# Optimization experiments

Measured on AMD Instinct MI355X. Metric: run time of the kernel, lower is better.

## Reference

```python
import jax, jax.numpy as jnp
import numpy as np
from jax import lax

N_QUBITS = 8
DIM = 256  # 2**8 amplitudes
NUM_BLOCKS = 16
DEPTH = 1
ALPHA = 0.5
BATCH = 512

# Z-sign tables: qubit 0 is the most-significant bit of the flattened state index
_bits = (np.arange(DIM)[:, None] >> (N_QUBITS - 1 - np.arange(N_QUBITS))) & 1  # (256, 8)
_SIGNS = jnp.asarray(1.0 - 2.0 * _bits, dtype=jnp.float32)  # (256, 8)
_pairs = [(i, j) for i in range(N_QUBITS) for j in range(i + 1, N_QUBITS)]
_PAIR_SIGNS = jnp.stack([_SIGNS[:, i] * _SIGNS[:, j] for (i, j) in _pairs], axis=1)  # (256, 28)


def _apply_ry(state, c, s, q):
    # state: (N, 256) real (RY and CNOT keep the state real); gate on qubit q
    dl, dr = 2 ** q, 2 ** (N_QUBITS - 1 - q)
    st = state.reshape(-1, dl, 2, dr)
    s0, s1 = st[:, :, 0, :], st[:, :, 1, :]
    c_, s_ = c[:, None, None], s[:, None, None]
    n0 = c_ * s0 - s_ * s1
    n1 = s_ * s0 + c_ * s1
    return jnp.stack([n0, n1], axis=2).reshape(-1, DIM)


def _apply_cnot_chain(state, i):
    # CNOT control=i, target=i+1 (adjacent qubits)
    dl, dr = 2 ** i, 2 ** (N_QUBITS - 2 - i)
    st = state.reshape(-1, dl, 2, 2, dr)
    c0 = st[:, :, 0]                  # control=0: unchanged
    c1 = st[:, :, 1][:, :, ::-1]      # control=1: flip target bit
    return jnp.stack([c0, c1], axis=2).reshape(-1, DIM)


def _quantum_map(theta):
    # theta: (N, 8) -> (N, 36) [Z_i expectations (8) then Z_i Z_j for i<j (28)]
    half = 0.5 * theta
    c, s = jnp.cos(half), jnp.sin(half)
    state = jnp.zeros((theta.shape[0], DIM), dtype=theta.dtype).at[:, 0].set(1.0)
    for q in range(N_QUBITS):
        state = _apply_ry(state, c[:, q], s[:, q], q)
    for _ in range(DEPTH):
        for i in range(N_QUBITS - 1):
            state = _apply_cnot_chain(state, i)
    p = state * state  # probabilities (state is real)
    single = p @ _SIGNS          # (N, 8)
    two_body = p @ _PAIR_SIGNS   # (N, 28)
    return jnp.concatenate([single, two_body], axis=1)


def _bn(x, g, b, m, v):
    # inference-mode BatchNorm2d, eps=1e-5
    inv = g / jnp.sqrt(v + 1e-5)
    return x * inv[None, :, None, None] + (b - m * inv)[None, :, None, None]


def _conv(x, w, b):
    y = lax.conv_general_dilated(x, w, (1, 1), 'SAME',
                                 dimension_numbers=('NCHW', 'OIHW', 'NCHW'))
    return y + b[None, :, None, None]


def _maxpool2(x):
    return lax.reduce_window(x, -jnp.inf, lax.max, (1, 1, 2, 2), (1, 1, 2, 2), 'VALID')


def setup_inputs() -> dict:
    key = jax.random.key(0)
    ks = jax.random.split(key, 8)
    f32 = jnp.float32
    return {
        'x': jax.random.normal(ks[0], (BATCH, 3, 64, 64), dtype=f32),
        'conv1_w': jax.random.normal(ks[1], (16, 3, 3, 3), dtype=f32) * 0.1,
        'conv1_b': jnp.zeros((16,), f32),
        'bn1_g': jnp.ones((16,), f32), 'bn1_b': jnp.zeros((16,), f32),
        'bn1_m': jnp.zeros((16,), f32), 'bn1_v': jnp.ones((16,), f32),
        'conv2_w': jax.random.normal(ks[2], (32, 16, 3, 3), dtype=f32) * 0.08,
        'conv2_b': jnp.zeros((32,), f32),
        'bn2_g': jnp.ones((32,), f32), 'bn2_b': jnp.zeros((32,), f32),
        'bn2_m': jnp.zeros((32,), f32), 'bn2_v': jnp.ones((32,), f32),
        'conv3_w': jax.random.normal(ks[3], (64, 32, 3, 3), dtype=f32) * 0.06,
        'conv3_b': jnp.zeros((64,), f32),
        'bn3_g': jnp.ones((64,), f32), 'bn3_b': jnp.zeros((64,), f32),
        'bn3_m': jnp.zeros((64,), f32), 'bn3_v': jnp.ones((64,), f32),
        'proj_w': jax.random.normal(ks[4], (NUM_BLOCKS, 256, N_QUBITS), dtype=f32) * 0.06,
        'proj_b': jnp.zeros((NUM_BLOCKS, N_QUBITS), f32),
        'cls_w': jax.random.normal(ks[5], (10, NUM_BLOCKS * 36), dtype=f32) * 0.04,
        'cls_b': jnp.zeros((10,), f32),
    }


def reference(x, conv1_w, conv1_b, bn1_g, bn1_b, bn1_m, bn1_v,
              conv2_w, conv2_b, bn2_g, bn2_b, bn2_m, bn2_v,
              conv3_w, conv3_b, bn3_g, bn3_b, bn3_m, bn3_v,
              proj_w, proj_b, cls_w, cls_b):
    h = _maxpool2(jax.nn.relu(_bn(_conv(x, conv1_w, conv1_b), bn1_g, bn1_b, bn1_m, bn1_v)))
    h = _maxpool2(jax.nn.relu(_bn(_conv(h, conv2_w, conv2_b), bn2_g, bn2_b, bn2_m, bn2_v)))
    h = _maxpool2(jax.nn.relu(_bn(_conv(h, conv3_w, conv3_b), bn3_g, bn3_b, bn3_m, bn3_v)))
    B = h.shape[0]
    feats = h.reshape(B, NUM_BLOCKS, 256)  # 16 chunks of 256
    z = jnp.einsum('bkc,kcd->bkd', feats, proj_w) + proj_b[None]  # (B, 16, 8)
    theta = ALPHA * jnp.tanh(z)
    q_out = _quantum_map(theta.reshape(B * NUM_BLOCKS, N_QUBITS))  # (B*16, 36)
    combined = q_out.reshape(B, NUM_BLOCKS * 36)
    return combined @ cls_w.T + cls_b
```

## Files before the change

### kernel.cpp

```cpp
#include <hip/hip_runtime.h>
#include <hip/hip_bf16.h>
#include <math.h>

typedef __attribute__((ext_vector_type(8))) short short8;
typedef __attribute__((ext_vector_type(4))) float f32x4;

__device__ __forceinline__ unsigned short f2bf(float f) {
    union { float f; unsigned u; } x; x.f = f;
    unsigned r = x.u + 0x7FFF + ((x.u >> 16) & 1);
    return (unsigned short)(r >> 16);
}

__device__ __forceinline__ short8 mk8(uint2 a, uint2 b) {
    union { uint2 u[2]; short8 s; } x;
    x.u[0] = a; x.u[1] = b;
    return x.s;
}

__device__ __forceinline__ short8 mk8u(unsigned a, unsigned b, unsigned c, unsigned d) {
    union { unsigned u[4]; short8 s; } x;
    x.u[0] = a; x.u[1] = b; x.u[2] = c; x.u[3] = d;
    return x.s;
}

__global__ void k_prep(const float* __restrict__ w2, const float* __restrict__ w3,
    const float* g2, const float* be2, const float* m2, const float* v2, const float* cb2,
    const float* g3, const float* be3, const float* m3, const float* v3, const float* cb3,
    const float* __restrict__ w1,
    const float* g1, const float* be1, const float* m1, const float* v1, const float* cb1,
    const float* __restrict__ pjw,
    unsigned short* __restrict__ wp2, unsigned short* __restrict__ wp3,
    unsigned short* __restrict__ wp1,
    float* __restrict__ cst2, float* __restrict__ cst3, float* __restrict__ cst1,
    float* __restrict__ pjwt)
{
    int tid = blockIdx.x * 256 + threadIdx.x;
    if (tid < 5120) {
        int j = tid & 7, lane = (tid >> 3) & 63, o = (tid >> 9) & 1, s = tid >> 10;
        int kl = ((lane >> 4) << 3) + j;
        int tp = s * 2 + (kl >> 4);
        int ic = kl & 15;
        int oc = o * 16 + (lane & 15);
        float val = (tp < 9) ? w2[(oc * 16 + ic) * 9 + tp] : 0.f;
        wp2[tid] = f2bf(val);
    } else if (tid < 23552) {
        int idx = tid - 5120;
        int j = idx & 7, lane = (idx >> 3) & 63, o = (idx >> 9) & 3, tap = idx >> 11;
        int ic = ((lane >> 4) << 3) + j;
        int oc = o * 16 + (lane & 15);
        wp3[idx] = f2bf(w3[(oc * 32 + ic) * 9 + tap]);
    } else if (tid < 23648) {
        int c = tid - 23552;
        if (c < 32) {
            float inv = g2[c] * rsqrtf(v2[c] + 1e-5f);
            cst2[c] = inv;
            cst2[32 + c] = (cb2[c] - m2[c]) * inv + be2[c];
        } else {
            int c3 = c - 32;
            float inv = g3[c3] * rsqrtf(v3[c3] + 1e-5f);
            cst3[c3] = inv;
            cst3[64 + c3] = (cb3[c3] - m3[c3]) * inv + be3[c3];
        }
    } else if (tid < 24672) {
        int idx = tid - 23648;
        int j = idx & 7, lane = (idx >> 3) & 63, s = (idx >> 9) & 1;
        int k = ((lane >> 4) << 3) + j;
        int oc = lane & 15;
        float val = 0.f;
        if (s == 0) {
            int tap = k >> 2, ic = k & 3;
            if (ic < 3) val = w1[(oc * 3 + ic) * 9 + tap];
        } else {
            if (k < 3) val = w1[(oc * 3 + k) * 9 + 8];
        }
        wp1[idx] = f2bf(val);
    } else if (tid < 24688) {
        int c = tid - 24672;
        float inv = g1[c] * rsqrtf(v1[c] + 1e-5f);
        cst1[c] = inv;
        cst1[16 + c] = (cb1[c] - m1[c]) * inv + be1[c];
    } else if (tid < 57456) {
        int idx = tid - 24688;
        int k = idx >> 11, d = (idx >> 8) & 7, c = idx & 255;
        pjwt[idx] = pjw[k * 2048 + c * 8 + d];
    }
}

__global__ __launch_bounds__(256, 2) void k_fused(
    const float* __restrict__ x,
    const unsigned short* __restrict__ wp1, const float* __restrict__ cst1,
    const unsigned short* __restrict__ wp2, const float* __restrict__ cst2,
    const unsigned short* __restrict__ wp3, const float* __restrict__ cst3,
    const float* __restrict__ pjwt, const float* __restrict__ pjb,
    const float* __restrict__ cw, const float* __restrict__ cbias,
    float* __restrict__ out)
{
    __shared__ __align__(16) unsigned char smem[62784];
    unsigned short* xs  = (unsigned short*)smem;
    unsigned short* h2t = (unsigned short*)smem;
    unsigned short* h1  = (unsigned short*)(smem + 25920);
    float* feats = (float*)(smem + 25920);
    float* czs   = (float*)(smem + 25920 + 17408);
    float* partl = czs + 128;

    int b = blockIdx.x, t = threadIdx.x;
    int lane = t & 63, w = t >> 6, q = lane >> 4, xl = lane & 15;
    const float* img = x + (size_t)b * 12288;

    short8 A10 = *(const short8*)(wp1 + (lane << 3));
    short8 A11 = *(const short8*)(wp1 + ((64 + lane) << 3));
    int t0 = 2 * q, t1 = 2 * q + 1;
    int dy0 = t0 / 3 - 1, dx0 = t0 % 3 - 1;
    int dy1 = t1 / 3 - 1, dx1 = t1 % 3 - 1;
    float inv1[4], bs1[4];
    #pragma unroll
    for (int reg = 0; reg < 4; ++reg) {
        inv1[reg] = cst1[q * 4 + reg];
        bs1[reg]  = cst1[16 + q * 4 + reg];
    }
    #pragma unroll 1
    for (int h = 0; h < 2; ++h) {
        if (h) __syncthreads();
        int y0 = h * 32 - 1;
        #pragma unroll 1
        for (int i = 0; i < 9; ++i) {
            int idx = t + i * 256;
            if (idx < 2244) {
                int y = idx / 66, xx = idx - y * 66;
                int gy = y0 + y, gx = xx - 1;
                float v0 = 0.f, v1 = 0.f, v2 = 0.f;
                if ((unsigned)gy < 64u && (unsigned)gx < 64u) {
                    const float* pb = img + gy * 64 + gx;
                    v0 = pb[0]; v1 = pb[4096]; v2 = pb[8192];
                }
                uint2 pk;
                pk.x = (unsigned)f2bf(v0) | ((unsigned)f2bf(v1) << 16);
                pk.y = (unsigned)f2bf(v2);
                ((uint2*)xs)[idx] = pk;
            }
        }
        __syncthreads();
        #pragma unroll 1
        for (int xT = 0; xT < 4; ++xT) {
            int xb = xT * 16 + xl + 1;
            float pv[4], vo[4];
            #pragma unroll
            for (int r = 0; r < 8; ++r) {
                int ly = w * 8 + r + 1;
                const uint2* base = (const uint2*)xs;
                uint2 ua = base[(ly + dy0) * 66 + xb + dx0];
                uint2 ub = base[(ly + dy1) * 66 + xb + dx1];
                uint2 uc = base[(ly + 1) * 66 + xb + 1];
                f32x4 acc = (f32x4){0.f, 0.f, 0.f, 0.f};
                acc = __builtin_amdgcn_mfma_f32_16x16x32_bf16(A10, mk8(ua, ub), acc, 0, 0, 0);
                acc = __builtin_amdgcn_mfma_f32_16x16x32_bf16(A11, mk8(uc, uc), acc, 0, 0, 0);
                #pragma unroll
                for (int reg = 0; reg < 4; ++reg) {
                    float val = fmaxf(acc[reg] * inv1[reg] + bs1[reg], 0.f);
                    if (r & 1) {
                        float vm = fmaxf(val, pv[reg]);
                        vo[reg] = fmaxf(vm, __shfl_xor(vm, 1, 64));
                    } else {
                        pv[reg] = val;
                    }
                }
                if ((r & 1) && !(lane & 1)) {
                    int py = h * 16 + w * 4 + (r >> 1);
                    int px = xT * 8 + (xl >> 1);
                    int pos = py * 32 + px;
                    unsigned u0 = (unsigned)f2bf(vo[0]) | ((unsigned)f2bf(vo[1]) << 16);
                    unsigned u1 = (unsigned)f2bf(vo[2]) | ((unsigned)f2bf(vo[3]) << 16);
                    unsigned* hp = (unsigned*)h1 + pos * 9 + q * 2;
                    hp[0] = u0; hp[1] = u1;
                }
            }
        }
    }
    __syncthreads();

    if (t < 68) {
        int y, xx;
        if (t < 18)      { y = 0;       xx = t; }
        else if (t < 36) { y = 17;      xx = t - 18; }
        else if (t < 52) { y = t - 35;  xx = 0; }
        else             { y = t - 51;  xx = 17; }
        uint4* p = (uint4*)(h2t + (y * 18 + xx) * 40);
        uint4 z = {0u, 0u, 0u, 0u};
        p[0] = z; p[1] = z; p[2] = z; p[3] = z; p[4] = z;
    }
    short8 A2[5][2];
    #pragma unroll
    for (int s = 0; s < 5; ++s)
        #pragma unroll
        for (int o = 0; o < 2; ++o)
            A2[s][o] = *(const short8*)(wp2 + (((s * 2 + o) * 64 + lane) << 3));
    int dyA[5], dxA[5];
    #pragma unroll
    for (int s = 0; s < 5; ++s) {
        int tp = s * 2 + (q >> 1); if (tp > 8) tp = 8;
        int d3 = tp / 3;
        dyA[s] = d3 - 1; dxA[s] = tp - d3 * 3 - 1;
    }
    #pragma unroll 1
    for (int rr = 0; rr < 2; ++rr) {
        f32x4 acc[4][2][2];
        #pragma unroll
        for (int r = 0; r < 4; ++r)
            #pragma unroll
            for (int xT = 0; xT < 2; ++xT)
                #pragma unroll
                for (int o = 0; o < 2; ++o)
                    acc[r][xT][o] = (f32x4){0.f, 0.f, 0.f, 0.f};
        #pragma unroll
        for (int r = 0; r < 4; ++r) {
            int ry = w * 8 + rr * 4 + r;
            #pragma unroll
            for (int xT = 0; xT < 2; ++xT) {
                int gxb = xT * 16 + xl;
                #pragma unroll
                for (int s = 0; s < 5; ++s) {
                    int gy = ry + dyA[s], gx = gxb + dxA[s];
                    bool ok = ((unsigned)gy < 32u) && ((unsigned)gx < 32u);
                    int pos = ok ? gy * 32 + gx : 0;
                    const unsigned* hp = (const unsigned*)h1 + pos * 9 + (q & 1) * 4;
                    unsigned u0 = hp[0], u1 = hp[1], u2 = hp[2], u3 = hp[3];
                    if (!ok) { u0 = 0; u1 = 0; u2 = 0; u3 = 0; }
                    short8 B = mk8u(u0, u1, u2, u3);
                    acc[r][xT][0] = __builtin_amdgcn_mfma_f32_16x16x32_bf16(A2[s][0], B, acc[r][xT][0], 0, 0, 0);
                    acc[r][xT][1] = __builtin_amdgcn_mfma_f32_16x16x32_bf16(A2[s][1], B, acc[r][xT][1], 0, 0, 0);
                }
            }
        }
        #pragma unroll
        for (int oT = 0; oT < 2; ++oT)
            #pragma unroll
            for (int rp = 0; rp < 2; ++rp)
                #pragma unroll
                for (int xT = 0; xT < 2; ++xT) {
                    float vo[4];
                    #pragma unroll
                    for (int reg = 0; reg < 4; ++reg) {
                        int oc = oT * 16 + q * 4 + reg;
                        float inv = cst2[oc], bs = cst2[32 + oc];
                        float v0 = fmaxf(acc[rp * 2][xT][oT][reg] * inv + bs, 0.f);
                        float v1 = fmaxf(acc[rp * 2 + 1][xT][oT][reg] * inv + bs, 0.f);
                        float vm = fmaxf(v0, v1);
                        vo[reg] = fmaxf(vm, __shfl_xor(vm, 1, 64));
                    }
                    if (!(lane & 1)) {
                        int py = w * 4 + rr * 2 + rp;
                        int px = xT * 8 + (xl >> 1);
                        int pos = (py + 1) * 18 + (px + 1);
                        unsigned u0 = (unsigned)f2bf(vo[0]) | ((unsigned)f2bf(vo[1]) << 16);
                        unsigned u1 = (unsigned)f2bf(vo[2]) | ((unsigned)f2bf(vo[3]) << 16);
                        unsigned* hp = (unsigned*)h2t + pos * 20 + oT * 8 + q * 2;
                        hp[0] = u0; hp[1] = u1;
                    }
                }
    }
    __syncthreads();

    #pragma unroll 1
    for (int op = 0; op < 2; ++op) {
        short8 A3[9][2];
        #pragma unroll
        for (int tap = 0; tap < 9; ++tap)
            #pragma unroll
            for (int tt = 0; tt < 2; ++tt)
                A3[tap][tt] = *(const short8*)(wp3 + (((tap * 4 + op * 2 + tt) * 64 + lane) << 3));
        f32x4 acc[4][2];
        #pragma unroll
        for (int r = 0; r < 4; ++r) {
            acc[r][0] = (f32x4){0.f, 0.f, 0.f, 0.f};
            acc[r][1] = (f32x4){0.f, 0.f, 0.f, 0.f};
        }
        #pragma unroll
        for (int r = 0; r < 4; ++r) {
            int ry = w * 4 + r + 1;
            #pragma unroll
            for (int tap = 0; tap < 9; ++tap) {
                int pos = (ry + tap / 3 - 1) * 18 + xl + (tap % 3);
                short8 B = *(const short8*)(h2t + pos * 40 + q * 8);
                acc[r][0] = __builtin_amdgcn_mfma_f32_16x16x32_bf16(A3[tap][0], B, acc[r][0], 0, 0, 0);
                acc[r][1] = __builtin_amdgcn_mfma_f32_16x16x32_bf16(A3[tap][1], B, acc[r][1], 0, 0, 0);
            }
        }
        #pragma unroll
        for (int tt = 0; tt < 2; ++tt)
            #pragma unroll
            for (int reg = 0; reg < 4; ++reg) {
                int oc = (op * 2 + tt) * 16 + q * 4 + reg;
                float inv = cst3[oc], bs = cst3[64 + oc];
                #pragma unroll
                for (int rp = 0; rp < 2; ++rp) {
                    float v0 = fmaxf(acc[rp * 2][tt][reg] * inv + bs, 0.f);
                    float v1 = fmaxf(acc[rp * 2 + 1][tt][reg] * inv + bs, 0.f);
                    float vm = fmaxf(v0, v1);
                    float vv = fmaxf(vm, __shfl_xor(vm, 1, 64));
                    if (!(lane & 1))
                        feats[oc * 68 + (w * 2 + rp) * 8 + (xl >> 1)] = vv;
                }
            }
    }
    __syncthreads();

    if (t < 128) {
        int k = t >> 3, d = t & 7;
        const float4* wrow = (const float4*)(pjwt + (k * 8 + d) * 256);
        float zacc = 0.f;
        #pragma unroll 4
        for (int i = 0; i < 64; ++i) {
            int c4 = (i + k) & 63;
            float4 wv = wrow[c4];
            const float* fp = &feats[(k * 4 + (c4 >> 4)) * 68 + 4 * (c4 & 15)];
            float4 fv = *(const float4*)fp;
            zacc = fmaf(wv.x, fv.x, zacc);
            zacc = fmaf(wv.y, fv.y, zacc);
            zacc = fmaf(wv.z, fv.z, zacc);
            zacc = fmaf(wv.w, fv.w, zacc);
        }
        float z = zacc + pjb[k * 8 + d];
        czs[k * 8 + d] = cosf(0.5f * tanhf(z));
    }
    __syncthreads();
    if (t < 160) {
        int k = t / 10, c = t - (t / 10) * 10;
        float cz[8];
        #pragma unroll
        for (int i = 0; i < 8; ++i) cz[i] = czs[k * 8 + i];
        const float* cwp = cw + c * 576 + k * 36;
        float s = 0.f;
        float pp = 1.f;
        #pragma unroll
        for (int i = 0; i < 8; ++i) { pp *= cz[i]; s = fmaf(pp, cwp[i], s); }
        int cnt = 8;
        #pragma unroll
        for (int i = 0; i < 8; ++i) {
            float p2 = 1.f;
            #pragma unroll
            for (int j = i + 1; j < 8; ++j) { p2 *= cz[j]; s = fmaf(p2, cwp[cnt++], s); }
        }
        partl[k * 10 + c] = s;
    }
    __syncthreads();
    if (t < 10) {
        float s = cbias[t];
        #pragma unroll
        for (int k = 0; k < 16; ++k) s += partl[k * 10 + t];
        out[b * 10 + t] = s;
    }
}

extern "C" void kernel_launch(void* const* d_in, const int* in_sizes, int n_in,
                              void* d_out, int out_size, void* d_ws, size_t ws_size,
                              hipStream_t stream) {
    const float* x     = (const float*)d_in[0];
    const float* c1w   = (const float*)d_in[1];
    const float* c1b   = (const float*)d_in[2];
    const float* b1g   = (const float*)d_in[3];
    const float* b1b   = (const float*)d_in[4];
    const float* b1m   = (const float*)d_in[5];
    const float* b1v   = (const float*)d_in[6];
    const float* c2w   = (const float*)d_in[7];
    const float* c2b   = (const float*)d_in[8];
    const float* b2g   = (const float*)d_in[9];
    const float* b2b   = (const float*)d_in[10];
    const float* b2m   = (const float*)d_in[11];
    const float* b2v   = (const float*)d_in[12];
    const float* c3w   = (const float*)d_in[13];
    const float* c3b   = (const float*)d_in[14];
    const float* b3g   = (const float*)d_in[15];
    const float* b3b   = (const float*)d_in[16];
    const float* b3m   = (const float*)d_in[17];
    const float* b3v   = (const float*)d_in[18];
    const float* pjw   = (const float*)d_in[19];
    const float* pjb   = (const float*)d_in[20];
    const float* cw    = (const float*)d_in[21];
    const float* cbias = (const float*)d_in[22];
    float* outp = (float*)d_out;

    unsigned char* prep = (unsigned char*)d_ws;
    unsigned short* wp2 = (unsigned short*)prep;
    unsigned short* wp3 = (unsigned short*)(prep + 16384);
    unsigned short* wp1 = (unsigned short*)(prep + 16384 + 36864);
    float* cst2 = (float*)(prep + 16384 + 36864 + 2048);
    float* cst3 = cst2 + 64;
    float* cst1 = cst3 + 128;
    float* pjwt = (float*)(prep + 16384 + 36864 + 2048 + 1024);

    k_prep<<<225, 256, 0, stream>>>(c2w, c3w, b2g, b2b, b2m, b2v, c2b,
                                    b3g, b3b, b3m, b3v, c3b,
                                    c1w, b1g, b1b, b1m, b1v, c1b, pjw,
                                    wp2, wp3, wp1, cst2, cst3, cst1, pjwt);
    k_fused<<<512, 256, 0, stream>>>(x, wp1, cst1, wp2, cst2, wp3, cst3,
                                     pjwt, pjb, cw, cbias, outp);
}
```

Measured before the change: 147.1 us.

## Double threads per block and split padded LDS activations into halves

The fused CNN kernel now runs 512 threads (8 waves) per image instead of 256. Each wave handles half the rows in conv1 and conv2, and in conv3 the output-channel halves are split across waves. The h1 and h2 activation buffers are re-laid out as two zero-padded halves, each 16 bytes per position, so conv2 no longer needs bounds checks or per-element selects when loading. This adds parallelism and latency hiding per image, but launch_bounds(512,4) limits registers per thread, which could cause spills given the large A2/A3 fragment arrays.

```diff
diff --git a/kernel.cpp b/kernel.cpp
--- a/kernel.cpp
+++ b/kernel.cpp
@@ -14,12 +14,6 @@
 __device__ __forceinline__ short8 mk8(uint2 a, uint2 b) {
     union { uint2 u[2]; short8 s; } x;
     x.u[0] = a; x.u[1] = b;
-    return x.s;
-}
-
-__device__ __forceinline__ short8 mk8u(unsigned a, unsigned b, unsigned c, unsigned d) {
-    union { unsigned u[4]; short8 s; } x;
-    x.u[0] = a; x.u[1] = b; x.u[2] = c; x.u[3] = d;
     return x.s;
 }
 
@@ -86,7 +80,7 @@
     }
 }
 
-__global__ __launch_bounds__(256, 2) void k_fused(
+__global__ __launch_bounds__(512, 4) void k_fused(
     const float* __restrict__ x,
     const unsigned short* __restrict__ wp1, const float* __restrict__ cst1,
     const unsigned short* __restrict__ wp2, const float* __restrict__ cst2,
@@ -95,17 +89,30 @@
     const float* __restrict__ cw, const float* __restrict__ cbias,
     float* __restrict__ out)
 {
-    __shared__ __align__(16) unsigned char smem[62784];
-    unsigned short* xs  = (unsigned short*)smem;
-    unsigned short* h2t = (unsigned short*)smem;
-    unsigned short* h1  = (unsigned short*)(smem + 25920);
-    float* feats = (float*)(smem + 25920);
-    float* czs   = (float*)(smem + 25920 + 17408);
+    __shared__ __align__(16) unsigned char smem[57728];
+    unsigned short* xs   = (unsigned short*)smem;
+    unsigned short* h2tA = (unsigned short*)smem;
+    unsigned short* h2tB = (unsigned short*)(smem + 10368);
+    unsigned short* h1A  = (unsigned short*)(smem + 20736);
+    unsigned short* h1B  = (unsigned short*)(smem + 39232);
+    float* feats = (float*)(smem + 20736);
+    float* czs   = (float*)(smem + 20736 + 17408);
     float* partl = czs + 128;
 
     int b = blockIdx.x, t = threadIdx.x;
     int lane = t & 63, w = t >> 6, q = lane >> 4, xl = lane & 15;
     const float* img = x + (size_t)b * 12288;
+
+    if (t < 264) {
+        int arr = t & 1, idx = t >> 1;
+        int y, xx;
+        if (idx < 34)       { y = 0;        xx = idx; }
+        else if (idx < 68)  { y = 33;       xx = idx - 34; }
+        else if (idx < 100) { y = idx - 67; xx = 0; }
+        else                { y = idx - 99; xx = 33; }
+        uint4 z = {0u, 0u, 0u, 0u};
+        *(uint4*)((arr ? h1B : h1A) + (y * 34 + xx) * 8) = z;
+    }
 
     short8 A10 = *(const short8*)(wp1 + (lane << 3));
     short8 A11 = *(const short8*)(wp1 + ((64 + lane) << 3));
@@ -118,13 +125,14 @@
         inv1[reg] = cst1[q * 4 + reg];
         bs1[reg]  = cst1[16 + q * 4 + reg];
     }
+    unsigned* h1w = (unsigned*)(q < 2 ? h1A : h1B);
     #pragma unroll 1
     for (int h = 0; h < 2; ++h) {
         if (h) __syncthreads();
         int y0 = h * 32 - 1;
         #pragma unroll 1
-        for (int i = 0; i < 9; ++i) {
-            int idx = t + i * 256;
+        for (int i = 0; i < 5; ++i) {
+            int idx = t + i * 512;
             if (idx < 2244) {
                 int y = idx / 66, xx = idx - y * 66;
                 int gy = y0 + y, gx = xx - 1;
@@ -145,8 +153,8 @@
             int xb = xT * 16 + xl + 1;
             float pv[4], vo[4];
             #pragma unroll
-            for (int r = 0; r < 8; ++r) {
-                int ly = w * 8 + r + 1;
+            for (int r = 0; r < 4; ++r) {
+                int ly = w * 4 + r + 1;
                 const uint2* base = (const uint2*)xs;
                 uint2 ua = base[(ly + dy0) * 66 + xb + dx0];
                 uint2 ub = base[(ly + dy1) * 66 + xb + dx1];
@@ -165,12 +173,12 @@
                     }
                 }
                 if ((r & 1) && !(lane & 1)) {
-                    int py = h * 16 + w * 4 + (r >> 1);
+                    int py = h * 16 + w * 2 + (r >> 1);
                     int px = xT * 8 + (xl >> 1);
-                    int pos = py * 32 + px;
+                    int pos = (py + 1) * 34 + (px + 1);
                     unsigned u0 = (unsigned)f2bf(vo[0]) | ((unsigned)f2bf(vo[1]) << 16);
                     unsigned u1 = (unsigned)f2bf(vo[2]) | ((unsigned)f2bf(vo[3]) << 16);
-                    unsigned* hp = (unsigned*)h1 + pos * 9 + q * 2;
+                    unsigned* hp = h1w + pos * 4 + (q & 1) * 2;
                     hp[0] = u0; hp[1] = u1;
                 }
             }
@@ -178,15 +186,20 @@
     }
     __syncthreads();
 
-    if (t < 68) {
+    if (t < 264) {
+        int idx = t >> 1, half = t & 1;
         int y, xx;
-        if (t < 18)      { y = 0;       xx = t; }
-        else if (t < 36) { y = 17;      xx = t - 18; }
-        else if (t < 52) { y = t - 35;  xx = 0; }
-        else             { y = t - 51;  xx = 17; }
-        uint4* p = (uint4*)(h2t + (y * 18 + xx) * 40);
-        uint4 z = {0u, 0u, 0u, 0u};
-        p[0] = z; p[1] = z; p[2] = z; p[3] = z; p[4] = z;
+        if (idx < 18)      { y = 0;        xx = idx; }
+        else if (idx < 36) { y = 17;       xx = idx - 18; }
+        else if (idx < 52) { y = idx - 35; xx = 0; }
+        else if (idx < 68) { y = idx - 51; xx = 17; }
+        else { y = -1; xx = 0; }
+        if (y >= 0) {
+            uint4 z = {0u, 0u, 0u, 0u};
+            int pos = y * 18 + xx;
+            *(uint4*)((half ? h2tB : h2tA) + pos * 16) = z;
+            *(uint4*)((half ? h2tB : h2tA) + pos * 16 + 8) = z;
+        }
     }
     short8 A2[5][2];
     #pragma unroll
@@ -201,8 +214,8 @@
         int d3 = tp / 3;
         dyA[s] = d3 - 1; dxA[s] = tp - d3 * 3 - 1;
     }
-    #pragma unroll 1
-    for (int rr = 0; rr < 2; ++rr) {
+    {
+        const unsigned short* h1r = (q & 1) ? h1B : h1A;
         f32x4 acc[4][2][2];
         #pragma unroll
         for (int r = 0; r < 4; ++r)
@@ -213,19 +226,14 @@
                     acc[r][xT][o] = (f32x4){0.f, 0.f, 0.f, 0.f};
         #pragma unroll
         for (int r = 0; r < 4; ++r) {
-            int ry = w * 8 + rr * 4 + r;
+            int ry = w * 4 + r;
             #pragma unroll
             for (int xT = 0; xT < 2; ++xT) {
                 int gxb = xT * 16 + xl;
                 #pragma unroll
                 for (int s = 0; s < 5; ++s) {
-                    int gy = ry + dyA[s], gx = gxb + dxA[s];
-                    bool ok = ((unsigned)gy < 32u) && ((unsigned)gx < 32u);
-                    int pos = ok ? gy * 32 + gx : 0;
-                    const unsigned* hp = (const unsigned*)h1 + pos * 9 + (q & 1) * 4;
-                    unsigned u0 = hp[0], u1 = hp[1], u2 = hp[2], u3 = hp[3];
-                    if (!ok) { u0 = 0; u1 = 0; u2 = 0; u3 = 0; }
-                    short8 B = mk8u(u0, u1, u2, u3);
+                    int pos = (ry + dyA[s] + 1) * 34 + (gxb + dxA[s] + 1);
+                    short8 B = *(const short8*)(h1r + pos * 8);
                     acc[r][xT][0] = __builtin_amdgcn_mfma_f32_16x16x32_bf16(A2[s][0], B, acc[r][xT][0], 0, 0, 0);
                     acc[r][xT][1] = __builtin_amdgcn_mfma_f32_16x16x32_bf16(A2[s][1], B, acc[r][xT][1], 0, 0, 0);
                 }
@@ -248,20 +256,21 @@
                         vo[reg] = fmaxf(vm, __shfl_xor(vm, 1, 64));
                     }
                     if (!(lane & 1)) {
-                        int py = w * 4 + rr * 2 + rp;
+                        int py = w * 2 + rp;
                         int px = xT * 8 + (xl >> 1);
                         int pos = (py + 1) * 18 + (px + 1);
                         unsigned u0 = (unsigned)f2bf(vo[0]) | ((unsigned)f2bf(vo[1]) << 16);
                         unsigned u1 = (unsigned)f2bf(vo[2]) | ((unsigned)f2bf(vo[3]) << 16);
-                        unsigned* hp = (unsigned*)h2t + pos * 20 + oT * 8 + q * 2;
+                        unsigned* hp = (unsigned*)(oT ? h2tB : h2tA) + pos * 8 + q * 2;
                         hp[0] = u0; hp[1] = u1;
                     }
                 }
     }
     __syncthreads();
 
-    #pragma unroll 1
-    for (int op = 0; op < 2; ++op) {
+    {
+        int op = w & 1, rg = w >> 1;
+        const unsigned short* h2r = (q < 2) ? h2tA : h2tB;
         short8 A3[9][2];
         #pragma unroll
         for (int tap = 0; tap < 9; ++tap)
@@ -276,11 +285,11 @@
         }
         #pragma unroll
         for (int r = 0; r < 4; ++r) {
-            int ry = w * 4 + r + 1;
+            int ry = rg * 4 + r + 1;
             #pragma unroll
             for (int tap = 0; tap < 9; ++tap) {
                 int pos = (ry + tap / 3 - 1) * 18 + xl + (tap % 3);
-                short8 B = *(const short8*)(h2t + pos * 40 + q * 8);
+                short8 B = *(const short8*)(h2r + pos * 16 + (q & 1) * 8);
                 acc[r][0] = __builtin_amdgcn_mfma_f32_16x16x32_bf16(A3[tap][0], B, acc[r][0], 0, 0, 0);
                 acc[r][1] = __builtin_amdgcn_mfma_f32_16x16x32_bf16(A3[tap][1], B, acc[r][1], 0, 0, 0);
             }
@@ -298,7 +307,7 @@
                     float vm = fmaxf(v0, v1);
                     float vv = fmaxf(vm, __shfl_xor(vm, 1, 64));
                     if (!(lane & 1))
-                        feats[oc * 68 + (w * 2 + rp) * 8 + (xl >> 1)] = vv;
+                        feats[oc * 68 + (rg * 2 + rp) * 8 + (xl >> 1)] = vv;
                 }
             }
     }
@@ -392,6 +401,6 @@
                                     b3g, b3b, b3m, b3v, c3b,
                                     c1w, b1g, b1b, b1m, b1v, c1b, pjw,
                                     wp2, wp3, wp1, cst2, cst3, cst1, pjwt);
-    k_fused<<<512, 256, 0, stream>>>(x, wp1, cst1, wp2, cst2, wp3, cst3,
+    k_fused<<<512, 512, 0, stream>>>(x, wp1, cst1, wp2, cst2, wp3, cst3,
                                      pjwt, pjb, cw, cbias, outp);
 }
```

Result: faster. 138.8 us (-5.7%).
